# Performance work log

Hardware: AMD Instinct MI355X
Metric: run time of the kernel (lower is better)

Reference implementation:

```python
import jax, jax.numpy as jnp
import numpy as np

# Config constants (match init_kwargs)
H = 1024   # hidden_size
F = 4096   # intermediate_size
E = 8      # num_moe_experts
K = 2      # moe_router_topk
S, B = 1024, 2  # seq_len, micro-batch


def setup_inputs() -> dict:
    key = jax.random.key(0)
    ks = jax.random.split(key, 6)
    return {
        "hidden_states": jax.random.normal(ks[0], (S, B, H), jnp.float32),
        "router_w": jax.random.normal(ks[1], (H, E), jnp.float32) * 0.02,
        "w1": jax.random.normal(ks[2], (E, H, F), jnp.float32) * 0.02,
        "b1": jax.random.normal(ks[3], (E, F), jnp.float32) * 0.02,
        "w2": jax.random.normal(ks[4], (E, F, H), jnp.float32) * 0.02,
        "b2": jax.random.normal(ks[5], (E, H), jnp.float32) * 0.02,
    }


def reference(hidden_states, router_w, w1, b1, w2, b2):
    S_, B_, H_ = hidden_states.shape
    x = hidden_states.reshape(-1, H_)                      # [N, H]
    N = x.shape[0]

    # --- TopKRouter (aux_loss routing): topk over logits, softmax over top-k logits ---
    logits = x @ router_w                                  # [N, E]
    top_logits, indices = jax.lax.top_k(logits, K)         # [N, K]
    scores = jax.nn.softmax(top_logits.astype(jnp.float32), axis=-1).astype(logits.dtype)

    # Combine weights [N, E]: scatter top-k scores into expert slots.
    combine = jnp.zeros((N, E), x.dtype).at[jnp.arange(N)[:, None], indices].add(scores)

    # --- Experts: per-expert GPTNeoXMLP (dense over all tokens; math-equivalent
    # to dispatch (token_permutation) + grouped GEMM + scatter_add combine
    # (token_unpermutation) with score weighting for topk>1) ---
    h = jax.nn.gelu(jnp.einsum('nh,ehf->enf', x, w1) + b1[:, None, :], approximate=False)
    y = jnp.einsum('enf,efh->enh', h, w2) + b2[:, None, :]  # [E, N, H]

    out = jnp.einsum('ne,enh->nh', combine, y)              # weighted combine
    return out.reshape(S_, B_, H_)
```

## Files before the change

kernel.cpp:

```cpp
#include <hip/hip_runtime.h>
#include <cmath>


#define H_DIM 1024
#define F_DIM 4096
#define E_NUM 8
#define N_TOK 2048
#define BK 32
#define MAX_SLOTS 5120
#define MAX_MT 40
#define G1_GRID (MAX_MT * 32)
#define G2_GRID (MAX_MT * 8 * 2)
#define CVT_BLKS 2048
#define WCHUNKS (E_NUM * H_DIM * F_DIM / 8)
#define XCHUNKS (N_TOK * H_DIM / 8)

typedef short s16x4 __attribute__((ext_vector_type(4)));
typedef short s16x8 __attribute__((ext_vector_type(8)));
typedef float f32x4 __attribute__((ext_vector_type(4)));
typedef __attribute__((address_space(3))) const unsigned short* lds_us;

__device__ __forceinline__ unsigned short f2bf(float f) {
  unsigned int u = __float_as_uint(f);
  u += 0x7fffu + ((u >> 16) & 1u);
  return (unsigned short)(u >> 16);
}

__device__ __forceinline__ void gload_lds16(const void* g, void* l) {
  __builtin_amdgcn_global_load_lds(
      (const __attribute__((address_space(1))) unsigned int*)g,
      (__attribute__((address_space(3))) unsigned int*)l, 16, 0, 0);
}

__device__ __forceinline__ int xcd_swz(int orig, int nwg) {
  const int cpx = nwg >> 3;
  return (orig & 7) * cpx + (orig >> 3);
}

__device__ __forceinline__ float fast_gelu(float v) {
  const float w = v * (1.0f + 0.044715f * v * v);
  const float t = __expf(-1.5957691216f * w);
  return v / (1.0f + t);
}

template<int OFS>
__device__ __forceinline__ s16x4 trread(lds_us p) {
  s16x4 r;
  asm volatile("ds_read_b64_tr_b16 %0, %1 offset:%2" : "=v"(r) : "v"(p), "i"(OFS));
  return r;
}

__device__ __forceinline__ void ld_b4(lds_us bp, s16x8 bb[4]) {
  s16x4 p0 = trread<0>(bp),    q0 = trread<512>(bp);
  s16x4 p1 = trread<1024>(bp), q1 = trread<1536>(bp);
  s16x4 p2 = trread<2048>(bp), q2 = trread<2560>(bp);
  s16x4 p3 = trread<3072>(bp), q3 = trread<3584>(bp);
  bb[0] = __builtin_shufflevector(p0, q0, 0, 1, 2, 3, 4, 5, 6, 7);
  bb[1] = __builtin_shufflevector(p1, q1, 0, 1, 2, 3, 4, 5, 6, 7);
  bb[2] = __builtin_shufflevector(p2, q2, 0, 1, 2, 3, 4, 5, 6, 7);
  bb[3] = __builtin_shufflevector(p3, q3, 0, 1, 2, 3, 4, 5, 6, 7);
}

__device__ __forceinline__ void cvt_stream(const float* __restrict__ in,
                                           unsigned short* __restrict__ out,
                                           int blk, int nblk, int nchunks) {
  const int step = nblk * 256;
#pragma unroll 8
  for (int c = blk * 256 + threadIdx.x; c < nchunks; c += step) {
    const size_t i = (size_t)c * 8;
    f32x4 a = __builtin_nontemporal_load((const f32x4*)(in + i));
    f32x4 b = __builtin_nontemporal_load((const f32x4*)(in + i + 4));
    s16x8 u;
#pragma unroll
    for (int j = 0; j < 4; ++j) { u[j] = (short)f2bf(a[j]); u[4 + j] = (short)f2bf(b[j]); }
    __builtin_nontemporal_store(u, (s16x8*)&out[i]);
  }
}

__global__ __launch_bounds__(256) void prep_k(
    const float* __restrict__ w1, unsigned short* __restrict__ wbf1,
    const float* __restrict__ x, unsigned short* __restrict__ xb,
    const float* __restrict__ rw, int* __restrict__ topk_e, float* __restrict__ topk_s) {
  const int b = blockIdx.x;
  const int t = threadIdx.x;
  if (b < CVT_BLKS) { cvt_stream(w1, wbf1, b, CVT_BLKS, WCHUNKS); return; }
  if (b < CVT_BLKS + 128) { cvt_stream(x, xb, b - CVT_BLKS, 128, XCHUNKS); return; }
  const int n = (b - CVT_BLKS - 128) * 4 + (t >> 6);
  const int l = t & 63;
  float part[E_NUM];
#pragma unroll
  for (int e = 0; e < E_NUM; ++e) part[e] = 0.f;
  const float* xr = x + (size_t)n * H_DIM;
  for (int h = l; h < H_DIM; h += 64) {
    const float xv = xr[h];
    const float* rwr = rw + h * E_NUM;
#pragma unroll
    for (int e = 0; e < E_NUM; ++e) part[e] += xv * rwr[e];
  }
#pragma unroll
  for (int e = 0; e < E_NUM; ++e) {
#pragma unroll
    for (int off = 32; off > 0; off >>= 1) part[e] += __shfl_down(part[e], off);
  }
  if (l == 0) {
    float v0 = -3.4e38f, v1 = -3.4e38f;
    int i0 = 0, i1 = 0;
#pragma unroll
    for (int e = 0; e < E_NUM; ++e) {
      float v = part[e];
      if (v > v0) { v1 = v0; i1 = i0; v0 = v; i0 = e; }
      else if (v > v1) { v1 = v; i1 = e; }
    }
    const float e1 = expf(v1 - v0);
    const float inv = 1.f / (1.f + e1);
    topk_e[2 * n] = i0; topk_e[2 * n + 1] = i1;
    topk_s[2 * n] = inv; topk_s[2 * n + 1] = e1 * inv;
  }
}

__global__ __launch_bounds__(256) void scatter_k(
    int* __restrict__ meta, const int* __restrict__ topk_e,
    int* __restrict__ slot_token, int* __restrict__ token_slots) {
  __shared__ int cnt[4][8];
  __shared__ int soff[9];
  __shared__ int scur[8];
  const int t = threadIdx.x;
  const int wv = t >> 6;
  if (t < 32) cnt[t >> 3][t & 7] = 0;
  if (t < 8) scur[t] = 0;
  __syncthreads();
  for (int a = t; a < N_TOK * 2; a += 256)
    atomicAdd(&cnt[wv][topk_e[a]], 1);
  __syncthreads();
  if (t == 0) {
    int acc = 0;
    for (int e = 0; e < E_NUM; ++e) {
      const int c = cnt[0][e] + cnt[1][e] + cnt[2][e] + cnt[3][e];
      soff[e] = acc;
      meta[8 + e] = acc;
      acc += ((c + 127) / 128) * 128;
    }
    soff[8] = acc;
    meta[16] = acc;
  }
  __syncthreads();
  for (int a = t; a < N_TOK * 2; a += 256) {
    const int e = topk_e[a];
    const int pos = atomicAdd(&scur[e], 1);
    const int slot = soff[e] + pos;
    slot_token[slot] = a >> 1;
    token_slots[a] = slot;
  }
}

#define KLANE(l) (((l) >> 3 & 3) * 8 + ((l) >> 5) * 4 + (((l) & 7) >> 1))

__global__ __launch_bounds__(256, 3) void gemm1_f(
    const unsigned short* __restrict__ xb, const unsigned short* __restrict__ wbf1,
    const float* __restrict__ b1, const int* __restrict__ meta,
    const int* __restrict__ slot_token, unsigned short* __restrict__ hbuf,
    const float* __restrict__ w2, unsigned short* __restrict__ wbf2) {
  __shared__ __align__(16) unsigned short Al[3 * 4096];
  __shared__ __align__(16) unsigned short Bl[3 * 4096];
  if (blockIdx.x >= G1_GRID) {
    cvt_stream(w2, wbf2, blockIdx.x - G1_GRID, CVT_BLKS, WCHUNKS);
    return;
  }
  const int total = meta[16];
  const int wgid = xcd_swz(blockIdx.x, G1_GRID);
  const int mt = wgid >> 5, nt = wgid & 31;
  const int m0 = mt * 128;
  if (m0 >= total) return;
  int exp = 0;
#pragma unroll
  for (int e = 1; e < E_NUM; ++e) if (m0 >= meta[8 + e]) exp = e;
  const int n0 = nt * 128;
  const int t = threadIdx.x, w = t >> 6, l = t & 63;
  const int wm = w >> 1, wn = w & 1, lr = l & 15, lg = l >> 4;

  const unsigned short* pA[2];
  const unsigned short* pB[2];
#pragma unroll
  for (int i = 0; i < 2; ++i) {
    const int q = w * 2 + i;
    const int row = q * 16 + (l >> 2);
    int tk = slot_token[m0 + row]; if (tk < 0) tk = 0;
    pA[i] = xb + (size_t)tk * H_DIM + (((l & 3) ^ ((l >> 3) & 3)) << 3);
    pB[i] = wbf1 + (size_t)exp * H_DIM * F_DIM + (size_t)KLANE(l) * F_DIM
            + n0 + q * 16 + (l & 1) * 8;
  }

  const f32x4 fzero = {0.f, 0.f, 0.f, 0.f};
  f32x4 acc[4][4];
#pragma unroll
  for (int a = 0; a < 4; ++a)
#pragma unroll
    for (int b = 0; b < 4; ++b) acc[a][b] = fzero;
  const int fofs = ((lg ^ ((lr >> 1) & 3)) << 3);

#define ISSUE1(Ad, Bd)                                                      \
  _Pragma("unroll") for (int i = 0; i < 2; ++i) {                           \
    gload_lds16(pA[i], (Ad) + (w * 2 + i) * 512); pA[i] += BK;              \
    gload_lds16(pB[i], (Bd) + (w * 2 + i) * 512); pB[i] += (size_t)BK * F_DIM; \
  }
#define MFMA1(Ac, Bc)                                                       \
  {                                                                         \
    lds_us bp = (lds_us)(Bc) + wn * 2048 + l * 4;                           \
    s16x8 af[4], bb[4];                                                     \
    _Pragma("unroll") for (int fm = 0; fm < 4; ++fm)                        \
      af[fm] = *(const s16x8*)&(Ac)[(wm * 64 + fm * 16 + lr) * 32 + fofs];  \
    ld_b4(bp, bb);                                                          \
    asm volatile("s_waitcnt lgkmcnt(0)" ::: "memory");                      \
    __builtin_amdgcn_sched_barrier(0);                                      \
    _Pragma("unroll") for (int fm = 0; fm < 4; ++fm)                        \
      _Pragma("unroll") for (int fn = 0; fn < 4; ++fn)                      \
        acc[fm][fn] = __builtin_amdgcn_mfma_f32_16x16x32_bf16(af[fm], bb[fn], acc[fm][fn], 0, 0, 0); \
  }

  const int NT = H_DIM / BK;
  ISSUE1(Al, Bl)
  ISSUE1(Al + 4096, Bl + 4096)
  int cur = 0;
  for (int kt = 0; kt < NT; ++kt) {
    if (kt + 1 < NT) asm volatile("s_waitcnt vmcnt(4)" ::: "memory");
    else             asm volatile("s_waitcnt vmcnt(0)" ::: "memory");
    __builtin_amdgcn_s_barrier();
    __builtin_amdgcn_sched_barrier(0);
    if (kt + 2 < NT) {
      int ib = cur + 2; if (ib >= 3) ib -= 3;
      ISSUE1(Al + ib * 4096, Bl + ib * 4096)
    }
    MFMA1(Al + cur * 4096, Bl + cur * 4096)
    ++cur; if (cur == 3) cur = 0;
  }

#pragma unroll
  for (int fn = 0; fn < 4; ++fn) {
    const int col = n0 + wn * 64 + fn * 16 + lr;
    const float bias = b1[exp * F_DIM + col];
#pragma unroll
    for (int fm = 0; fm < 4; ++fm) {
      const int rbase = m0 + wm * 64 + fm * 16 + lg * 4;
#pragma unroll
      for (int i = 0; i < 4; ++i) {
        hbuf[(size_t)(rbase + i) * F_DIM + col] = f2bf(fast_gelu(acc[fm][fn][i] + bias));
      }
    }
  }
}

__global__ __launch_bounds__(256, 3) void gemm2_f(
    const unsigned short* __restrict__ hbuf, const unsigned short* __restrict__ wbf2,
    const int* __restrict__ meta, unsigned short* __restrict__ yb) {
  __shared__ __align__(16) unsigned short Al[3 * 4096];
  __shared__ __align__(16) unsigned short Bl[3 * 4096];
  const int total = meta[16];
  const int c = blockIdx.x & 7;
  const int r = blockIdx.x >> 3;
  const int nt = c;
  const int ks = r & 1;
  const int mt = r >> 1;
  const int m0 = mt * 128;
  if (m0 >= total) return;
  int exp = 0;
#pragma unroll
  for (int e = 1; e < E_NUM; ++e) if (m0 >= meta[8 + e]) exp = e;
  const int n0 = nt * 128;
  const int k0 = ks * 2048;
  const int t = threadIdx.x, w = t >> 6, l = t & 63;
  const int wm = w >> 1, wn = w & 1, lr = l & 15, lg = l >> 4;

  const unsigned short* pA[2];
  const unsigned short* pB[2];
#pragma unroll
  for (int i = 0; i < 2; ++i) {
    const int q = w * 2 + i;
    const int row = q * 16 + (l >> 2);
    pA[i] = hbuf + (size_t)(m0 + row) * F_DIM + k0 + (((l & 3) ^ ((l >> 3) & 3)) << 3);
    pB[i] = wbf2 + (size_t)exp * F_DIM * H_DIM + (size_t)(k0 + KLANE(l)) * H_DIM
            + n0 + q * 16 + (l & 1) * 8;
  }

  const f32x4 fzero = {0.f, 0.f, 0.f, 0.f};
  f32x4 acc[4][4];
#pragma unroll
  for (int a = 0; a < 4; ++a)
#pragma unroll
    for (int b = 0; b < 4; ++b) acc[a][b] = fzero;
  const int fofs = ((lg ^ ((lr >> 1) & 3)) << 3);

#define ISSUE2(Ad, Bd)                                                      \
  _Pragma("unroll") for (int i = 0; i < 2; ++i) {                           \
    gload_lds16(pA[i], (Ad) + (w * 2 + i) * 512); pA[i] += BK;              \
    gload_lds16(pB[i], (Bd) + (w * 2 + i) * 512); pB[i] += (size_t)BK * H_DIM; \
  }

  const int NT = 2048 / BK;
  ISSUE2(Al, Bl)
  ISSUE2(Al + 4096, Bl + 4096)
  int cur = 0;
  for (int kt = 0; kt < NT; ++kt) {
    if (kt + 1 < NT) asm volatile("s_waitcnt vmcnt(4)" ::: "memory");
    else             asm volatile("s_waitcnt vmcnt(0)" ::: "memory");
    __builtin_amdgcn_s_barrier();
    __builtin_amdgcn_sched_barrier(0);
    if (kt + 2 < NT) {
      int ib = cur + 2; if (ib >= 3) ib -= 3;
      ISSUE2(Al + ib * 4096, Bl + ib * 4096)
    }
    MFMA1(Al + cur * 4096, Bl + cur * 4096)
    ++cur; if (cur == 3) cur = 0;
  }

  unsigned short* yk = yb + (size_t)ks * MAX_SLOTS * H_DIM;
#pragma unroll
  for (int fn = 0; fn < 4; ++fn) {
    const int col = n0 + wn * 64 + fn * 16 + lr;
#pragma unroll
    for (int fm = 0; fm < 4; ++fm) {
      const int rbase = m0 + wm * 64 + fm * 16 + lg * 4;
#pragma unroll
      for (int i = 0; i < 4; ++i) {
        yk[(size_t)(rbase + i) * H_DIM + col] = f2bf(acc[fm][fn][i]);
      }
    }
  }
}

__global__ __launch_bounds__(256) void combine_k(
    const unsigned short* __restrict__ yb, const float* __restrict__ b2,
    const int* __restrict__ token_slots, const int* __restrict__ topk_e,
    const float* __restrict__ topk_s, float* __restrict__ out) {
  const int tok = blockIdx.x;
  const int c4 = threadIdx.x * 4;
  const int sl0 = token_slots[2 * tok], sl1 = token_slots[2 * tok + 1];
  const float s0 = topk_s[2 * tok], s1 = topk_s[2 * tok + 1];
  const int e0 = topk_e[2 * tok], e1 = topk_e[2 * tok + 1];
  const unsigned short* y1p = yb + (size_t)MAX_SLOTS * H_DIM;
  ushort4 a0 = *(const ushort4*)(yb  + (size_t)sl0 * H_DIM + c4);
  ushort4 a1 = *(const ushort4*)(y1p + (size_t)sl0 * H_DIM + c4);
  ushort4 d0 = *(const ushort4*)(yb  + (size_t)sl1 * H_DIM + c4);
  ushort4 d1 = *(const ushort4*)(y1p + (size_t)sl1 * H_DIM + c4);
  f32x4 ba = *(const f32x4*)(b2 + e0 * H_DIM + c4);
  f32x4 bd = *(const f32x4*)(b2 + e1 * H_DIM + c4);
  const unsigned short* ap0 = &a0.x; const unsigned short* ap1 = &a1.x;
  const unsigned short* dp0 = &d0.x; const unsigned short* dp1 = &d1.x;
  f32x4 o;
#pragma unroll
  for (int j = 0; j < 4; ++j) {
    const float ya = __uint_as_float((unsigned)ap0[j] << 16) + __uint_as_float((unsigned)ap1[j] << 16) + ba[j];
    const float yd = __uint_as_float((unsigned)dp0[j] << 16) + __uint_as_float((unsigned)dp1[j] << 16) + bd[j];
    o[j] = s0 * ya + s1 * yd;
  }
  *(f32x4*)(out + (size_t)tok * H_DIM + c4) = o;
}

extern "C" void kernel_launch(void* const* d_in, const int* in_sizes, int n_in,
                              void* d_out, int out_size, void* d_ws, size_t ws_size,
                              hipStream_t stream) {
  const float* x  = (const float*)d_in[0];
  const float* rw = (const float*)d_in[1];
  const float* w1 = (const float*)d_in[2];
  const float* b1 = (const float*)d_in[3];
  const float* w2 = (const float*)d_in[4];
  const float* b2 = (const float*)d_in[5];
  float* out = (float*)d_out;
  char* ws = (char*)d_ws;

  int*   meta        = (int*)ws;
  int*   topk_e      = (int*)(ws + 4096);
  float* topk_s      = (float*)(ws + 36864);
  int*   slot_token  = (int*)(ws + 69632);
  int*   token_slots = (int*)(ws + 102400);
  unsigned short* xb   = (unsigned short*)(ws + (1ull << 20));
  unsigned short* hbuf = (unsigned short*)(ws + (6ull << 20));
  unsigned short* wbf2 = (unsigned short*)(ws + (46ull << 20));
  unsigned short* wbf1 = (unsigned short*)(ws + (110ull << 20));
  unsigned short* yb   = wbf1;

  hipMemsetAsync(meta, 0, 256, stream);
  hipMemsetAsync(slot_token, 0xFF, MAX_SLOTS * sizeof(int), stream);

  prep_k<<<CVT_BLKS + 128 + 512, 256, 0, stream>>>(w1, wbf1, x, xb, rw, topk_e, topk_s);
  scatter_k<<<1, 256, 0, stream>>>(meta, topk_e, slot_token, token_slots);
  gemm1_f<<<G1_GRID + CVT_BLKS, 256, 0, stream>>>(xb, wbf1, b1, meta, slot_token, hbuf, w2, wbf2);
  gemm2_f<<<G2_GRID, 256, 0, stream>>>(hbuf, wbf2, meta, yb);
  combine_k<<<N_TOK, 256, 0, stream>>>(yb, b2, token_slots, topk_e, topk_s, out);
}
```

Baseline: 261.7 us.

## Fuse fp32-to-bf16 weight conversion into expert GEMM B-tile loads

Drops the separate full-weight fp32-to-bf16 conversion passes for w1 and w2. The GEMM kernels now load fp32 weight tiles into registers, pack them to bf16 with v_cvt_pk_bf16_f32, and write them into a padded double-buffered LDS layout. The A tiles keep their async LDS loads. This removes the 128MB fp32 read plus 64MB bf16 write-and-reread of the weights. In exchange, each routed tile reads fp32 weights, about twice the bytes of bf16, and tiles of the same expert re-read them. Register-staged loads can also expose more latency than the direct-to-LDS path. The gemm1 block mapping was also changed to a simple XCD-grouped scheme.

```diff
diff --git a/kernel.cpp b/kernel.cpp
--- a/kernel.cpp
+++ b/kernel.cpp
@@ -11,8 +11,6 @@
 #define MAX_MT 40
 #define G1_GRID (MAX_MT * 32)
 #define G2_GRID (MAX_MT * 8 * 2)
-#define CVT_BLKS 2048
-#define WCHUNKS (E_NUM * H_DIM * F_DIM / 8)
 #define XCHUNKS (N_TOK * H_DIM / 8)
 
 typedef short s16x4 __attribute__((ext_vector_type(4)));
@@ -32,15 +30,16 @@
       (__attribute__((address_space(3))) unsigned int*)l, 16, 0, 0);
 }
 
-__device__ __forceinline__ int xcd_swz(int orig, int nwg) {
-  const int cpx = nwg >> 3;
-  return (orig & 7) * cpx + (orig >> 3);
-}
-
 __device__ __forceinline__ float fast_gelu(float v) {
   const float w = v * (1.0f + 0.044715f * v * v);
   const float t = __expf(-1.5957691216f * w);
   return v / (1.0f + t);
+}
+
+__device__ __forceinline__ unsigned int pk_bf16(float lo, float hi) {
+  unsigned int r;
+  asm("v_cvt_pk_bf16_f32 %0, %1, %2" : "=v"(r) : "v"(lo), "v"(hi));
+  return r;
 }
 
 template<int OFS>
@@ -52,40 +51,35 @@
 
 __device__ __forceinline__ void ld_b4(lds_us bp, s16x8 bb[4]) {
   s16x4 p0 = trread<0>(bp),    q0 = trread<512>(bp);
-  s16x4 p1 = trread<1024>(bp), q1 = trread<1536>(bp);
-  s16x4 p2 = trread<2048>(bp), q2 = trread<2560>(bp);
-  s16x4 p3 = trread<3072>(bp), q3 = trread<3584>(bp);
+  s16x4 p1 = trread<1040>(bp), q1 = trread<1552>(bp);
+  s16x4 p2 = trread<2080>(bp), q2 = trread<2592>(bp);
+  s16x4 p3 = trread<3120>(bp), q3 = trread<3632>(bp);
   bb[0] = __builtin_shufflevector(p0, q0, 0, 1, 2, 3, 4, 5, 6, 7);
   bb[1] = __builtin_shufflevector(p1, q1, 0, 1, 2, 3, 4, 5, 6, 7);
   bb[2] = __builtin_shufflevector(p2, q2, 0, 1, 2, 3, 4, 5, 6, 7);
   bb[3] = __builtin_shufflevector(p3, q3, 0, 1, 2, 3, 4, 5, 6, 7);
 }
 
-__device__ __forceinline__ void cvt_stream(const float* __restrict__ in,
-                                           unsigned short* __restrict__ out,
-                                           int blk, int nblk, int nchunks) {
-  const int step = nblk * 256;
-#pragma unroll 8
-  for (int c = blk * 256 + threadIdx.x; c < nchunks; c += step) {
-    const size_t i = (size_t)c * 8;
-    f32x4 a = __builtin_nontemporal_load((const f32x4*)(in + i));
-    f32x4 b = __builtin_nontemporal_load((const f32x4*)(in + i + 4));
-    s16x8 u;
-#pragma unroll
-    for (int j = 0; j < 4; ++j) { u[j] = (short)f2bf(a[j]); u[4 + j] = (short)f2bf(b[j]); }
-    __builtin_nontemporal_store(u, (s16x8*)&out[i]);
-  }
-}
-
 __global__ __launch_bounds__(256) void prep_k(
-    const float* __restrict__ w1, unsigned short* __restrict__ wbf1,
     const float* __restrict__ x, unsigned short* __restrict__ xb,
     const float* __restrict__ rw, int* __restrict__ topk_e, float* __restrict__ topk_s) {
   const int b = blockIdx.x;
   const int t = threadIdx.x;
-  if (b < CVT_BLKS) { cvt_stream(w1, wbf1, b, CVT_BLKS, WCHUNKS); return; }
-  if (b < CVT_BLKS + 128) { cvt_stream(x, xb, b - CVT_BLKS, 128, XCHUNKS); return; }
-  const int n = (b - CVT_BLKS - 128) * 4 + (t >> 6);
+  if (b < 128) {
+    const int step = 128 * 256;
+#pragma unroll 4
+    for (int c = b * 256 + t; c < XCHUNKS; c += step) {
+      const size_t i = (size_t)c * 8;
+      f32x4 a = *(const f32x4*)(x + i);
+      f32x4 d = *(const f32x4*)(x + i + 4);
+      s16x8 u;
+#pragma unroll
+      for (int j = 0; j < 4; ++j) { u[j] = (short)f2bf(a[j]); u[4 + j] = (short)f2bf(d[j]); }
+      *(s16x8*)&xb[i] = u;
+    }
+    return;
+  }
+  const int n = (b - 128) * 4 + (t >> 6);
   const int l = t & 63;
   float part[E_NUM];
 #pragma unroll
@@ -153,22 +147,16 @@
   }
 }
 
-#define KLANE(l) (((l) >> 3 & 3) * 8 + ((l) >> 5) * 4 + (((l) & 7) >> 1))
-
 __global__ __launch_bounds__(256, 3) void gemm1_f(
-    const unsigned short* __restrict__ xb, const unsigned short* __restrict__ wbf1,
+    const unsigned short* __restrict__ xb, const float* __restrict__ w1,
     const float* __restrict__ b1, const int* __restrict__ meta,
-    const int* __restrict__ slot_token, unsigned short* __restrict__ hbuf,
-    const float* __restrict__ w2, unsigned short* __restrict__ wbf2) {
+    const int* __restrict__ slot_token, unsigned short* __restrict__ hbuf) {
   __shared__ __align__(16) unsigned short Al[3 * 4096];
-  __shared__ __align__(16) unsigned short Bl[3 * 4096];
-  if (blockIdx.x >= G1_GRID) {
-    cvt_stream(w2, wbf2, blockIdx.x - G1_GRID, CVT_BLKS, WCHUNKS);
-    return;
-  }
+  __shared__ __align__(16) char Bl[2 * 8 * 1040];
   const int total = meta[16];
-  const int wgid = xcd_swz(blockIdx.x, G1_GRID);
-  const int mt = wgid >> 5, nt = wgid & 31;
+  const int c = blockIdx.x & 7;
+  const int j = blockIdx.x >> 3;
+  const int mt = j >> 2, nt = c * 4 + (j & 3);
   const int m0 = mt * 128;
   if (m0 >= total) return;
   int exp = 0;
@@ -179,16 +167,16 @@
   const int wm = w >> 1, wn = w & 1, lr = l & 15, lg = l >> 4;
 
   const unsigned short* pA[2];
-  const unsigned short* pB[2];
 #pragma unroll
   for (int i = 0; i < 2; ++i) {
     const int q = w * 2 + i;
     const int row = q * 16 + (l >> 2);
     int tk = slot_token[m0 + row]; if (tk < 0) tk = 0;
     pA[i] = xb + (size_t)tk * H_DIM + (((l & 3) ^ ((l >> 3) & 3)) << 3);
-    pB[i] = wbf1 + (size_t)exp * H_DIM * F_DIM + (size_t)KLANE(l) * F_DIM
-            + n0 + q * 16 + (l & 1) * 8;
-  }
+  }
+  const int krow = t >> 3, cg = t & 7;
+  const float* pB = w1 + (size_t)exp * H_DIM * F_DIM + (size_t)krow * F_DIM + n0 + cg * 16;
+  const int wb = cg * 1040 + ((krow >> 2) & 1) * 512 + (krow >> 3) * 128 + (krow & 3) * 32;
 
   const f32x4 fzero = {0.f, 0.f, 0.f, 0.f};
   f32x4 acc[4][4];
@@ -198,14 +186,22 @@
     for (int b = 0; b < 4; ++b) acc[a][b] = fzero;
   const int fofs = ((lg ^ ((lr >> 1) & 3)) << 3);
 
-#define ISSUE1(Ad, Bd)                                                      \
+#define ISSUEA1(Ad)                                                         \
   _Pragma("unroll") for (int i = 0; i < 2; ++i) {                           \
     gload_lds16(pA[i], (Ad) + (w * 2 + i) * 512); pA[i] += BK;              \
-    gload_lds16(pB[i], (Bd) + (w * 2 + i) * 512); pB[i] += (size_t)BK * F_DIM; \
-  }
+  }
+#define LOADB1(v)                                                           \
+  { _Pragma("unroll") for (int q_ = 0; q_ < 4; ++q_) v[q_] = *(const f32x4*)(pB + q_ * 4); \
+    pB += (size_t)BK * F_DIM; }
+#define CVTB1(v, Bd)                                                        \
+  { int4 u0, u1;                                                            \
+    u0.x = (int)pk_bf16(v[0][0], v[0][1]); u0.y = (int)pk_bf16(v[0][2], v[0][3]); \
+    u0.z = (int)pk_bf16(v[1][0], v[1][1]); u0.w = (int)pk_bf16(v[1][2], v[1][3]); \
+    u1.x = (int)pk_bf16(v[2][0], v[2][1]); u1.y = (int)pk_bf16(v[2][2], v[2][3]); \
+    u1.z = (int)pk_bf16(v[3][0], v[3][1]); u1.w = (int)pk_bf16(v[3][2], v[3][3]); \
+    *(int4*)((Bd) + wb) = u0; *(int4*)((Bd) + wb + 16) = u1; }
 #define MFMA1(Ac, Bc)                                                       \
-  {                                                                         \
-    lds_us bp = (lds_us)(Bc) + wn * 2048 + l * 4;                           \
+  { lds_us bp = (lds_us)((Bc) + wn * 4160) + l * 4;                         \
     s16x8 af[4], bb[4];                                                     \
     _Pragma("unroll") for (int fm = 0; fm < 4; ++fm)                        \
       af[fm] = *(const s16x8*)&(Ac)[(wm * 64 + fm * 16 + lr) * 32 + fofs];  \
@@ -217,21 +213,36 @@
         acc[fm][fn] = __builtin_amdgcn_mfma_f32_16x16x32_bf16(af[fm], bb[fn], acc[fm][fn], 0, 0, 0); \
   }
 
+  unsigned short *a0 = Al, *a1 = Al + 4096, *a2 = Al + 8192;
+  char *bl0 = Bl, *bl1 = Bl + 8320;
+  f32x4 vP[4], vQ[4];
   const int NT = H_DIM / BK;
-  ISSUE1(Al, Bl)
-  ISSUE1(Al + 4096, Bl + 4096)
-  int cur = 0;
-  for (int kt = 0; kt < NT; ++kt) {
-    if (kt + 1 < NT) asm volatile("s_waitcnt vmcnt(4)" ::: "memory");
-    else             asm volatile("s_waitcnt vmcnt(0)" ::: "memory");
+  LOADB1(vP) ISSUEA1(a0)
+  LOADB1(vQ) ISSUEA1(a1)
+  asm volatile("s_waitcnt vmcnt(6)" ::: "memory");
+  CVTB1(vP, bl0)
+  asm volatile("s_waitcnt lgkmcnt(0)" ::: "memory");
+  __builtin_amdgcn_s_barrier();
+  for (int it = 0; it < NT / 2; ++it) {
+    const bool has2 = it < NT / 2 - 1;
+    if (has2) { ISSUEA1(a2) LOADB1(vP) }
+    if (has2) asm volatile("s_waitcnt vmcnt(6)" ::: "memory");
+    else      asm volatile("s_waitcnt vmcnt(0)" ::: "memory");
+    CVTB1(vQ, bl1)
+    MFMA1(a0, bl0)
+    asm volatile("s_waitcnt lgkmcnt(0)" ::: "memory");
     __builtin_amdgcn_s_barrier();
-    __builtin_amdgcn_sched_barrier(0);
-    if (kt + 2 < NT) {
-      int ib = cur + 2; if (ib >= 3) ib -= 3;
-      ISSUE1(Al + ib * 4096, Bl + ib * 4096)
-    }
-    MFMA1(Al + cur * 4096, Bl + cur * 4096)
-    ++cur; if (cur == 3) cur = 0;
+    { unsigned short* tmp = a0; a0 = a1; a1 = a2; a2 = tmp; }
+    if (has2) { ISSUEA1(a2) LOADB1(vQ) }
+    if (has2) asm volatile("s_waitcnt vmcnt(6)" ::: "memory");
+    else      asm volatile("s_waitcnt vmcnt(0)" ::: "memory");
+    if (has2) { CVTB1(vP, bl0) }
+    MFMA1(a0, bl1)
+    if (has2) {
+      asm volatile("s_waitcnt lgkmcnt(0)" ::: "memory");
+      __builtin_amdgcn_s_barrier();
+    }
+    { unsigned short* tmp = a0; a0 = a1; a1 = a2; a2 = tmp; }
   }
 
 #pragma unroll
@@ -250,10 +261,10 @@
 }
 
 __global__ __launch_bounds__(256, 3) void gemm2_f(
-    const unsigned short* __restrict__ hbuf, const unsigned short* __restrict__ wbf2,
+    const unsigned short* __restrict__ hbuf, const float* __restrict__ w2,
     const int* __restrict__ meta, unsigned short* __restrict__ yb) {
   __shared__ __align__(16) unsigned short Al[3 * 4096];
-  __shared__ __align__(16) unsigned short Bl[3 * 4096];
+  __shared__ __align__(16) char Bl[2 * 8 * 1040];
   const int total = meta[16];
   const int c = blockIdx.x & 7;
   const int r = blockIdx.x >> 3;
@@ -271,15 +282,15 @@
   const int wm = w >> 1, wn = w & 1, lr = l & 15, lg = l >> 4;
 
   const unsigned short* pA[2];
-  const unsigned short* pB[2];
 #pragma unroll
   for (int i = 0; i < 2; ++i) {
     const int q = w * 2 + i;
     const int row = q * 16 + (l >> 2);
     pA[i] = hbuf + (size_t)(m0 + row) * F_DIM + k0 + (((l & 3) ^ ((l >> 3) & 3)) << 3);
-    pB[i] = wbf2 + (size_t)exp * F_DIM * H_DIM + (size_t)(k0 + KLANE(l)) * H_DIM
-            + n0 + q * 16 + (l & 1) * 8;
-  }
+  }
+  const int krow = t >> 3, cg = t & 7;
+  const float* pB = w2 + (size_t)exp * F_DIM * H_DIM + (size_t)(k0 + krow) * H_DIM + n0 + cg * 16;
+  const int wb = cg * 1040 + ((krow >> 2) & 1) * 512 + (krow >> 3) * 128 + (krow & 3) * 32;
 
   const f32x4 fzero = {0.f, 0.f, 0.f, 0.f};
   f32x4 acc[4][4];
@@ -289,27 +300,44 @@
     for (int b = 0; b < 4; ++b) acc[a][b] = fzero;
   const int fofs = ((lg ^ ((lr >> 1) & 3)) << 3);
 
-#define ISSUE2(Ad, Bd)                                                      \
+#define ISSUEA2(Ad)                                                         \
   _Pragma("unroll") for (int i = 0; i < 2; ++i) {                           \
     gload_lds16(pA[i], (Ad) + (w * 2 + i) * 512); pA[i] += BK;              \
-    gload_lds16(pB[i], (Bd) + (w * 2 + i) * 512); pB[i] += (size_t)BK * H_DIM; \
-  }
-
+  }
+#define LOADB2(v)                                                           \
+  { _Pragma("unroll") for (int q_ = 0; q_ < 4; ++q_) v[q_] = *(const f32x4*)(pB + q_ * 4); \
+    pB += (size_t)BK * H_DIM; }
+
+  unsigned short *a0 = Al, *a1 = Al + 4096, *a2 = Al + 8192;
+  char *bl0 = Bl, *bl1 = Bl + 8320;
+  f32x4 vP[4], vQ[4];
   const int NT = 2048 / BK;
-  ISSUE2(Al, Bl)
-  ISSUE2(Al + 4096, Bl + 4096)
-  int cur = 0;
-  for (int kt = 0; kt < NT; ++kt) {
-    if (kt + 1 < NT) asm volatile("s_waitcnt vmcnt(4)" ::: "memory");
-    else             asm volatile("s_waitcnt vmcnt(0)" ::: "memory");
+  LOADB2(vP) ISSUEA2(a0)
+  LOADB2(vQ) ISSUEA2(a1)
+  asm volatile("s_waitcnt vmcnt(6)" ::: "memory");
+  CVTB1(vP, bl0)
+  asm volatile("s_waitcnt lgkmcnt(0)" ::: "memory");
+  __builtin_amdgcn_s_barrier();
+  for (int it = 0; it < NT / 2; ++it) {
+    const bool has2 = it < NT / 2 - 1;
+    if (has2) { ISSUEA2(a2) LOADB2(vP) }
+    if (has2) asm volatile("s_waitcnt vmcnt(6)" ::: "memory");
+    else      asm volatile("s_waitcnt vmcnt(0)" ::: "memory");
+    CVTB1(vQ, bl1)
+    MFMA1(a0, bl0)
+    asm volatile("s_waitcnt lgkmcnt(0)" ::: "memory");
     __builtin_amdgcn_s_barrier();
-    __builtin_amdgcn_sched_barrier(0);
-    if (kt + 2 < NT) {
-      int ib = cur + 2; if (ib >= 3) ib -= 3;
-      ISSUE2(Al + ib * 4096, Bl + ib * 4096)
-    }
-    MFMA1(Al + cur * 4096, Bl + cur * 4096)
-    ++cur; if (cur == 3) cur = 0;
+    { unsigned short* tmp = a0; a0 = a1; a1 = a2; a2 = tmp; }
+    if (has2) { ISSUEA2(a2) LOADB2(vQ) }
+    if (has2) asm volatile("s_waitcnt vmcnt(6)" ::: "memory");
+    else      asm volatile("s_waitcnt vmcnt(0)" ::: "memory");
+    if (has2) { CVTB1(vP, bl0) }
+    MFMA1(a0, bl1)
+    if (has2) {
+      asm volatile("s_waitcnt lgkmcnt(0)" ::: "memory");
+      __builtin_amdgcn_s_barrier();
+    }
+    { unsigned short* tmp = a0; a0 = a1; a1 = a2; a2 = tmp; }
   }
 
   unsigned short* yk = yb + (size_t)ks * MAX_SLOTS * H_DIM;
@@ -374,16 +402,14 @@
   int*   token_slots = (int*)(ws + 102400);
   unsigned short* xb   = (unsigned short*)(ws + (1ull << 20));
   unsigned short* hbuf = (unsigned short*)(ws + (6ull << 20));
-  unsigned short* wbf2 = (unsigned short*)(ws + (46ull << 20));
-  unsigned short* wbf1 = (unsigned short*)(ws + (110ull << 20));
-  unsigned short* yb   = wbf1;
+  unsigned short* yb   = (unsigned short*)(ws + (46ull << 20));
 
   hipMemsetAsync(meta, 0, 256, stream);
   hipMemsetAsync(slot_token, 0xFF, MAX_SLOTS * sizeof(int), stream);
 
-  prep_k<<<CVT_BLKS + 128 + 512, 256, 0, stream>>>(w1, wbf1, x, xb, rw, topk_e, topk_s);
+  prep_k<<<128 + 512, 256, 0, stream>>>(x, xb, rw, topk_e, topk_s);
   scatter_k<<<1, 256, 0, stream>>>(meta, topk_e, slot_token, token_slots);
-  gemm1_f<<<G1_GRID + CVT_BLKS, 256, 0, stream>>>(xb, wbf1, b1, meta, slot_token, hbuf, w2, wbf2);
-  gemm2_f<<<G2_GRID, 256, 0, stream>>>(hbuf, wbf2, meta, yb);
+  gemm1_f<<<G1_GRID, 256, 0, stream>>>(xb, w1, b1, meta, slot_token, hbuf);
+  gemm2_f<<<G2_GRID, 256, 0, stream>>>(hbuf, w2, meta, yb);
   combine_k<<<N_TOK, 256, 0, stream>>>(yb, b2, token_slots, topk_e, topk_s, out);
 }
```

Result: faster. 227.9 us (-12.9%).
